# Optimization experiments

Measured on AMD Instinct MI355X. Metric: run time of the kernel, lower is better.

The kernel has to match this reference:

```python
import jax, jax.numpy as jnp
import numpy as np

B, S, D = 2, 2048, 1024
H = 16
HD = D // H  # head_dim = 64


def _xavier(key, shape):
    fan_out, fan_in = shape
    bound = jnp.sqrt(6.0 / (fan_in + fan_out))
    return jax.random.uniform(key, shape, jnp.float32, -bound, bound)


def setup_inputs() -> dict:
    key = jax.random.key(0)
    kx, kqkv, ko = jax.random.split(key, 3)
    x = jax.random.normal(kx, (B, S, D), jnp.float32)
    # torch nn.Linear stores weight as [out, in]; we keep that layout and use x @ W.T
    W_qkv = _xavier(kqkv, (3 * D, D))
    b_qkv = jnp.zeros((3 * D,), jnp.float32)
    W_o = _xavier(ko, (D, D))
    b_o = jnp.zeros((D,), jnp.float32)
    return {"x": x, "W_qkv": W_qkv, "b_qkv": b_qkv, "W_o": W_o, "b_o": b_o}


def reference(x, W_qkv, b_qkv, W_o, b_o):
    b, s, d = x.shape
    h, hd = H, HD
    # qkv projection: [b, s, 3d]
    qkv = jnp.einsum("bsd,ed->bse", x, W_qkv) + b_qkv
    # [b, s, h, 3*hd] -> [b, h, s, 3*hd]
    qkv = qkv.reshape(b, s, h, 3 * hd).transpose(0, 2, 1, 3)
    q, k, v = jnp.split(qkv, 3, axis=-1)
    scale = 1.0 / jnp.sqrt(jnp.asarray(hd, x.dtype))
    logits = jnp.einsum("bhqd,bhkd->bhqk", q, k) * scale
    attn = jax.nn.softmax(logits, axis=-1)
    values = jnp.einsum("bhqk,bhkd->bhqd", attn, v)
    values = values.transpose(0, 2, 1, 3).reshape(b, s, d)
    return jnp.einsum("bsd,ed->bse", values, W_o) + b_o
```

## Files before the change

### kernel.cpp

```cpp
#include <hip/hip_runtime.h>

typedef unsigned short u16;
typedef __attribute__((ext_vector_type(8))) short bf16x8;
typedef __attribute__((ext_vector_type(4))) float f32x4;
typedef __attribute__((ext_vector_type(16))) float f32x16;
typedef __attribute__((ext_vector_type(4))) unsigned short u16x4;

__device__ __forceinline__ u16 f2bf(float f) {
    unsigned u = __float_as_uint(f);
    u = u + 0x7FFFu + ((u >> 16) & 1u);
    return (u16)(u >> 16);
}

__device__ __forceinline__ void gload16(const void* g, void* l) {
    __builtin_amdgcn_global_load_lds(
        (const __attribute__((address_space(1))) unsigned int*)g,
        (__attribute__((address_space(3))) unsigned int*)l,
        16, 0, 0);
}

__device__ __forceinline__ f32x4 mfma16(bf16x8 a, bf16x8 b, f32x4 c) {
    return __builtin_amdgcn_mfma_f32_16x16x32_bf16(a, b, c, 0, 0, 0);
}
__device__ __forceinline__ f32x16 mfma32(bf16x8 a, bf16x8 b, f32x16 c) {
    return __builtin_amdgcn_mfma_f32_32x32x16_bf16(a, b, c, 0, 0, 0);
}

__global__ __launch_bounds__(256) void cvt_all(const float* __restrict__ x,
                                               const float* __restrict__ wqkv,
                                               const float* __restrict__ wo,
                                               u16* __restrict__ dst) {
    int i = blockIdx.x * 256 + threadIdx.x;
    float4 v;
    if (i < 1048576)       v = ((const float4*)x)[i];
    else if (i < 1835008)  v = ((const float4*)wqkv)[i - 1048576];
    else                   v = ((const float4*)wo)[i - 1835008];
    u16x4 o = { f2bf(v.x), f2bf(v.y), f2bf(v.z), f2bf(v.w) };
    ((u16x4*)dst)[i] = o;
}

template <int BM, int BN, bool OUT_BF16>
__global__ __launch_bounds__(256) void gemm_bt(const u16* __restrict__ A,
                                               const u16* __restrict__ Bm,
                                               const float* __restrict__ bias,
                                               void* __restrict__ Cp,
                                               int M, int N, int K) {
    constexpr int FM = BM / 32, FN = BN / 32;
    __shared__ u16 As[BM * 64];
    __shared__ u16 Bs[BN * 64];
    const int tid = threadIdx.x, lane = tid & 63, wave = tid >> 6;
    const int wr = wave >> 1, wc = wave & 1;
    const int l15 = lane & 15, l4 = lane >> 4;

    const int nx = gridDim.x, nwg = nx * gridDim.y;
    const int id = blockIdx.y * nx + blockIdx.x;
    const int wg = (id & 7) * (nwg >> 3) + (id >> 3);
    const int m0 = (wg / nx) * BM, n0 = (wg % nx) * BN;

    f32x4 zero = {0.f, 0.f, 0.f, 0.f};
    f32x4 acc[FM][FN];
#pragma unroll
    for (int m = 0; m < FM; ++m)
#pragma unroll
        for (int n = 0; n < FN; ++n) acc[m][n] = zero;

    const int nt = K >> 6;
    for (int t = 0; t < nt; ++t) {
#pragma unroll
        for (int i = 0; i < BM / 32; ++i) {
            int c = i * 256 + tid;
            int r = c >> 3, kc = (c & 7) ^ (r & 7);
            gload16(A + (size_t)(m0 + r) * K + t * 64 + kc * 8,
                    As + (i * 256 + wave * 64) * 8);
        }
#pragma unroll
        for (int i = 0; i < BN / 32; ++i) {
            int c = i * 256 + tid;
            int r = c >> 3, kc = (c & 7) ^ (r & 7);
            gload16(Bm + (size_t)(n0 + r) * K + t * 64 + kc * 8,
                    Bs + (i * 256 + wave * 64) * 8);
        }
        __syncthreads();
#pragma unroll
        for (int kk = 0; kk < 2; ++kk) {
            bf16x8 af[FM], bfr[FN];
#pragma unroll
            for (int m = 0; m < FM; ++m) {
                int row = wr * (BM / 2) + m * 16 + l15;
                int ch = (kk * 4 + l4) ^ (row & 7);
                af[m] = *(const bf16x8*)((const char*)As + row * 128 + ch * 16);
            }
#pragma unroll
            for (int n = 0; n < FN; ++n) {
                int row = wc * (BN / 2) + n * 16 + l15;
                int ch = (kk * 4 + l4) ^ (row & 7);
                bfr[n] = *(const bf16x8*)((const char*)Bs + row * 128 + ch * 16);
            }
#pragma unroll
            for (int m = 0; m < FM; ++m)
#pragma unroll
                for (int n = 0; n < FN; ++n)
                    acc[m][n] = mfma16(af[m], bfr[n], acc[m][n]);
        }
        __syncthreads();
    }
    float bv[FN];
#pragma unroll
    for (int n = 0; n < FN; ++n) bv[n] = bias[n0 + wc * (BN / 2) + n * 16 + l15];
#pragma unroll
    for (int m = 0; m < FM; ++m) {
#pragma unroll
        for (int j = 0; j < 4; ++j) {
            size_t row = (size_t)(m0 + wr * (BM / 2) + m * 16 + l4 * 4 + j);
#pragma unroll
            for (int n = 0; n < FN; ++n) {
                int col = n0 + wc * (BN / 2) + n * 16 + l15;
                float v = acc[m][n][j] + bv[n];
                if (OUT_BF16)
                    ((u16*)Cp)[row * (size_t)N + col] = f2bf(v);
                else
                    ((float*)Cp)[row * (size_t)N + col] = v;
            }
        }
    }
}

__global__ __launch_bounds__(512) void gemm256(const u16* __restrict__ A,
                                               const u16* __restrict__ Bm,
                                               const float* __restrict__ bias,
                                               u16* __restrict__ Cp,
                                               int M, int N, int K) {
    __shared__ __align__(16) char lds[131072];
    const int tid = threadIdx.x, lane = tid & 63, wave = tid >> 6;
    const int wr = wave >> 2, wc = wave & 3;
    const int l15 = lane & 15, l4 = lane >> 4;

    const int nx = gridDim.x, nwg = nx * gridDim.y;
    const int id = blockIdx.y * nx + blockIdx.x;
    const int wg = (id & 7) * (nwg >> 3) + (id >> 3);
    const int m0 = (wg / nx) * 256, n0 = (wg % nx) * 256;

    const u16* asrc[2][2];
    const u16* bsrc[2][2];
#pragma unroll
    for (int q = 0; q < 2; ++q)
#pragma unroll
        for (int r = 0; r < 2; ++r) {
            int c = r * 512 + tid;
            int lr = c >> 3;
            int kc = (c & 7) ^ (lr & 7);
            asrc[q][r] = A  + (size_t)(m0 + lr + (lr & 64) + q * 64) * K + kc * 8;
            bsrc[q][r] = Bm + (size_t)(n0 + lr + (lr & 96) + q * 32) * K + kc * 8;
        }
    const int sd0 = wave * 1024;
    const int sd1 = 8192 + wave * 1024;

    const int roA = (wr * 64 + l15) * 128;
    const int roB = (wc * 32 + l15) * 128;
    int ch16[2];
#pragma unroll
    for (int kk = 0; kk < 2; ++kk) ch16[kk] = ((kk * 4 + l4) ^ (l15 & 7)) * 16;

    f32x4 zero = {0.f, 0.f, 0.f, 0.f};
    f32x4 acc[2][2][4][2];
#pragma unroll
    for (int a = 0; a < 2; ++a)
#pragma unroll
        for (int b = 0; b < 2; ++b)
#pragma unroll
            for (int c = 0; c < 4; ++c)
#pragma unroll
                for (int d = 0; d < 2; ++d) acc[a][b][c][d] = zero;

#define STG_A(q, tt) { char* rb = lds + (((tt) & 1) * 32768) + (q) * 16384;          \
        gload16(asrc[q][0] + (size_t)(tt) * 64, rb + sd0);                            \
        gload16(asrc[q][1] + (size_t)(tt) * 64, rb + sd1); }
#define STG_B(q, tt) { char* rb = lds + 65536 + (((tt) & 1) * 32768) + (q) * 16384;  \
        gload16(bsrc[q][0] + (size_t)(tt) * 64, rb + sd0);                            \
        gload16(bsrc[q][1] + (size_t)(tt) * 64, rb + sd1); }
#define MFMA_PH(MH, NH) {                                                             \
        __builtin_amdgcn_s_setprio(1);                                                \
        _Pragma("unroll")                                                             \
        for (int fm = 0; fm < 4; ++fm)                                                \
            _Pragma("unroll")                                                         \
            for (int fn = 0; fn < 2; ++fn)                                            \
                _Pragma("unroll")                                                     \
                for (int kk = 0; kk < 2; ++kk)                                        \
                    acc[MH][NH][fm][fn] =                                             \
                        mfma16(af[fm][kk], bfr[NH][fn][kk], acc[MH][NH][fm][fn]);     \
        __builtin_amdgcn_s_setprio(0); }

    STG_A(0, 0); STG_B(0, 0); STG_A(1, 0); STG_B(1, 0);
    asm volatile("s_waitcnt vmcnt(4)" ::: "memory");
    asm volatile("s_barrier" ::: "memory");

    bf16x8 af[4][2], bfr[2][2][2];
    const int nt = K >> 6;
    for (int t = 0; t < nt; ++t) {
        const char* Ab = lds + (t & 1) * 32768;
        const char* Bb = lds + 65536 + (t & 1) * 32768;
#pragma unroll
        for (int fm = 0; fm < 4; ++fm)
#pragma unroll
            for (int kk = 0; kk < 2; ++kk)
                af[fm][kk] = *(const bf16x8*)(Ab + roA + fm * 2048 + ch16[kk]);
#pragma unroll
        for (int fn = 0; fn < 2; ++fn)
#pragma unroll
            for (int kk = 0; kk < 2; ++kk)
                bfr[0][fn][kk] = *(const bf16x8*)(Bb + roB + fn * 2048 + ch16[kk]);
        if (t < nt - 1) STG_A(0, t + 1);
        asm volatile("s_barrier" ::: "memory");
        MFMA_PH(0, 0);
        asm volatile("s_barrier" ::: "memory");
#pragma unroll
        for (int fn = 0; fn < 2; ++fn)
#pragma unroll
            for (int kk = 0; kk < 2; ++kk)
                bfr[1][fn][kk] = *(const bf16x8*)(Bb + 16384 + roB + fn * 2048 + ch16[kk]);
        if (t < nt - 1) STG_B(0, t + 1);
        asm volatile("s_barrier" ::: "memory");
        MFMA_PH(0, 1);
        if (t < nt - 1) asm volatile("s_waitcnt vmcnt(4)" ::: "memory");
        else            asm volatile("s_waitcnt vmcnt(0)" ::: "memory");
        asm volatile("s_barrier" ::: "memory");
#pragma unroll
        for (int fm = 0; fm < 4; ++fm)
#pragma unroll
            for (int kk = 0; kk < 2; ++kk)
                af[fm][kk] = *(const bf16x8*)(Ab + 16384 + roA + fm * 2048 + ch16[kk]);
        if (t < nt - 1) STG_A(1, t + 1);
        asm volatile("s_barrier" ::: "memory");
        MFMA_PH(1, 0);
        asm volatile("s_barrier" ::: "memory");
        if (t < nt - 1) STG_B(1, t + 1);
        asm volatile("s_barrier" ::: "memory");
        MFMA_PH(1, 1);
        if (t < nt - 1) asm volatile("s_waitcnt vmcnt(4)" ::: "memory");
        asm volatile("s_barrier" ::: "memory");
    }
#undef STG_A
#undef STG_B
#undef MFMA_PH

    float bv[2][2];
#pragma unroll
    for (int nh = 0; nh < 2; ++nh)
#pragma unroll
        for (int fn = 0; fn < 2; ++fn)
            bv[nh][fn] = bias[n0 + wc * 64 + nh * 32 + fn * 16 + l15];
#pragma unroll
    for (int mh = 0; mh < 2; ++mh)
#pragma unroll
        for (int fm = 0; fm < 4; ++fm)
#pragma unroll
            for (int j = 0; j < 4; ++j) {
                size_t row = (size_t)(m0 + wr * 128 + mh * 64 + fm * 16 + l4 * 4 + j);
#pragma unroll
                for (int nh = 0; nh < 2; ++nh)
#pragma unroll
                    for (int fn = 0; fn < 2; ++fn) {
                        int col = n0 + wc * 64 + nh * 32 + fn * 16 + l15;
                        Cp[row * (size_t)N + col] =
                            f2bf(acc[mh][nh][fm][fn][j] + bv[nh][fn]);
                    }
            }
}

__global__ __launch_bounds__(256) void transpose_v(const u16* __restrict__ qkv,
                                                   u16* __restrict__ Vt) {
    __shared__ u16 tle[64][65];
    const int s0 = blockIdx.x * 64, h = blockIdx.y, b = blockIdx.z;
    const int tid = threadIdx.x;
#pragma unroll
    for (int i = 0; i < 16; ++i) {
        int idx = i * 256 + tid;
        int sk = idx >> 6, d = idx & 63;
        tle[sk][d] = qkv[(size_t)(b * 2048 + s0 + sk) * 3072 + h * 192 + 128 + d];
    }
    __syncthreads();
#pragma unroll
    for (int i = 0; i < 16; ++i) {
        int idx = i * 256 + tid;
        int d = idx >> 6, sk = idx & 63;
        Vt[((size_t)(b * 16 + h) * 64 + d) * 2048 + s0 + sk] = tle[sk][d];
    }
}

__global__ __launch_bounds__(512, 4) void attn_kernel(const u16* __restrict__ qkv,
                                                      const u16* __restrict__ Vt,
                                                      u16* __restrict__ vals) {
    __shared__ __align__(16) char lds[65536];
    const int qt = blockIdx.x, h = blockIdx.y, b = blockIdx.z;
    const int tid = threadIdx.x, lane = tid & 63, wave = tid >> 6;
    const int gtid = tid & 255, qsub = wave & 3, kvh = wave >> 2;
    const int l31 = lane & 31, hi = lane >> 5;
    const float S2E = 0.18033688f;

    const u16* qbase = qkv + (size_t)(b * 2048 + qt * 128 + qsub * 32 + l31) * 3072 + h * 192;
    bf16x8 Qf[4];
#pragma unroll
    for (int ks = 0; ks < 4; ++ks) {
        bf16x8 q = *(const bf16x8*)(qbase + ks * 16 + hi * 8);
#pragma unroll
        for (int j = 0; j < 8; ++j) {
            float f = __uint_as_float(((unsigned)(u16)q[j]) << 16) * S2E;
            q[j] = (short)f2bf(f);
        }
        Qf[ks] = q;
    }

    bf16x8 ones;
#pragma unroll
    for (int j = 0; j < 8; ++j) ones[j] = (short)0x3F80;

    const u16* kp[2];
    const u16* vp[2];
    int dst[2];
#pragma unroll
    for (int i = 0; i < 2; ++i) {
        int c = i * 256 + gtid;
        int fi = c >> 6, dl = c & 63;
        int mm = fi >> 2, ks = fi & 3;
        int row = mm * 32 + (dl & 31);
        int col = ks * 16 + (dl >> 5) * 8;
        kp[i] = qkv + (size_t)(b * 2048 + kvh * 1024 + row) * 3072 + h * 192 + 64 + col;
        vp[i] = Vt + ((size_t)((b * 16 + h) * 64 + row)) * 2048 + kvh * 1024 + col;
        dst[i] = fi * 512;
    }
    u16* Kst = (u16*)lds + kvh * 8192;
    u16* Vst = (u16*)lds + 16384 + kvh * 8192;

    f32x16 accO[2], accL;
#pragma unroll
    for (int md = 0; md < 2; ++md)
#pragma unroll
        for (int r = 0; r < 16; ++r) accO[md][r] = 0.f;
#pragma unroll
    for (int r = 0; r < 16; ++r) accL[r] = 0.f;

    const char* KsL = (const char*)Kst + lane * 16;
    const char* VsL = (const char*)Vst + lane * 16;

#pragma unroll
    for (int i = 0; i < 2; ++i) gload16(kp[i], Kst + dst[i]);
#pragma unroll
    for (int i = 0; i < 2; ++i) gload16(vp[i], Vst + dst[i]);
#pragma unroll
    for (int i = 0; i < 2; ++i) { kp[i] += 64 * 3072; vp[i] += 64; }

    for (int t = 0; t < 16; ++t) {
        if (t < 15) {
            u16* kd = Kst + ((t + 1) & 1) * 4096;
            u16* vd = Vst + ((t + 1) & 1) * 4096;
#pragma unroll
            for (int i = 0; i < 2; ++i) gload16(kp[i], kd + dst[i]);
#pragma unroll
            for (int i = 0; i < 2; ++i) gload16(vp[i], vd + dst[i]);
#pragma unroll
            for (int i = 0; i < 2; ++i) { kp[i] += 64 * 3072; vp[i] += 64; }
            asm volatile("s_waitcnt vmcnt(4)" ::: "memory");
        } else {
            asm volatile("s_waitcnt vmcnt(0)" ::: "memory");
        }
        asm volatile("s_barrier" ::: "memory");

        const char* Kb = KsL + (t & 1) * 8192;
        const char* Vb = VsL + (t & 1) * 8192;

        f32x16 sc[2];
        __builtin_amdgcn_s_setprio(1);
#pragma unroll
        for (int m = 0; m < 2; ++m) {
            f32x16 c;
#pragma unroll
            for (int r = 0; r < 16; ++r) c[r] = 0.f;
#pragma unroll
            for (int ks = 0; ks < 4; ++ks) {
                bf16x8 kf = *(const bf16x8*)(Kb + (m * 4 + ks) * 1024);
                c = mfma32(kf, Qf[ks], c);
            }
            sc[m] = c;
        }
        __builtin_amdgcn_s_setprio(0);

#pragma unroll
        for (int m = 0; m < 2; ++m)
#pragma unroll
            for (int r = 0; r < 16; ++r)
                sc[m][r] = exp2f(sc[m][r]);

        bf16x8 Pf[4];
#pragma unroll
        for (int m = 0; m < 2; ++m) {
            unsigned W0[4], W1[4];
#pragma unroll
            for (int g = 0; g < 4; ++g) {
                asm("v_cvt_pk_bf16_f32 %0, %1, %2"
                    : "=v"(W0[g]) : "v"(sc[m][4 * g + 0]), "v"(sc[m][4 * g + 1]));
                asm("v_cvt_pk_bf16_f32 %0, %1, %2"
                    : "=v"(W1[g]) : "v"(sc[m][4 * g + 2]), "v"(sc[m][4 * g + 3]));
            }
#pragma unroll
            for (int kpair = 0; kpair < 2; ++kpair) {
                unsigned xa = W0[2 * kpair], ya = W0[2 * kpair + 1];
                unsigned xb = W1[2 * kpair], yb = W1[2 * kpair + 1];
                asm volatile("v_permlane32_swap_b32 %0, %1" : "+v"(xa), "+v"(ya));
                asm volatile("v_permlane32_swap_b32 %0, %1" : "+v"(xb), "+v"(yb));
                union { unsigned w[4]; bf16x8 v; } u;
                u.w[0] = xa; u.w[1] = xb; u.w[2] = ya; u.w[3] = yb;
                Pf[2 * m + kpair] = u.v;
            }
        }

        __builtin_amdgcn_s_setprio(1);
#pragma unroll
        for (int md = 0; md < 2; ++md) {
            f32x16 c = accO[md];
#pragma unroll
            for (int ks = 0; ks < 4; ++ks) {
                bf16x8 vf = *(const bf16x8*)(Vb + (md * 4 + ks) * 1024);
                c = mfma32(vf, Pf[ks], c);
            }
            accO[md] = c;
        }
#pragma unroll
        for (int ks = 0; ks < 4; ++ks)
            accL = mfma32(ones, Pf[ks], accL);
        __builtin_amdgcn_s_setprio(0);

        asm volatile("s_barrier" ::: "memory");
    }

    float lt = accL[0];

    float* MO = (float*)lds;
    float* ML = (float*)(lds + 32768);
    __syncthreads();
    if (kvh == 1) {
#pragma unroll
        for (int md = 0; md < 2; ++md)
#pragma unroll
            for (int g = 0; g < 4; ++g) {
                f32x4 w = { accO[md][4 * g + 0], accO[md][4 * g + 1],
                            accO[md][4 * g + 2], accO[md][4 * g + 3] };
                *(f32x4*)&MO[(qsub * 64 + lane) * 32 + md * 16 + 4 * g] = w;
            }
        ML[qsub * 64 + lane] = lt;
    }
    __syncthreads();
    if (kvh == 0) {
        float inv = 1.f / (lt + ML[qsub * 64 + lane]);
        size_t rowoff = (size_t)(b * 2048 + qt * 128 + qsub * 32 + l31) * 1024 + h * 64;
#pragma unroll
        for (int md = 0; md < 2; ++md)
#pragma unroll
            for (int g = 0; g < 4; ++g) {
                f32x4 w = *(const f32x4*)&MO[(qsub * 64 + lane) * 32 + md * 16 + 4 * g];
                u16x4 o = { f2bf((accO[md][4 * g + 0] + w[0]) * inv),
                            f2bf((accO[md][4 * g + 1] + w[1]) * inv),
                            f2bf((accO[md][4 * g + 2] + w[2]) * inv),
                            f2bf((accO[md][4 * g + 3] + w[3]) * inv) };
                *(u16x4*)(vals + rowoff + md * 32 + 8 * g + 4 * hi) = o;
            }
    }
}

extern "C" void kernel_launch(void* const* d_in, const int* in_sizes, int n_in,
                              void* d_out, int out_size, void* d_ws, size_t ws_size,
                              hipStream_t stream) {
    const float* x    = (const float*)d_in[0];
    const float* Wqkv = (const float*)d_in[1];
    const float* bqkv = (const float*)d_in[2];
    const float* Wo   = (const float*)d_in[3];
    const float* bo   = (const float*)d_in[4];
    float* out = (float*)d_out;

    char* ws = (char*)d_ws;
    u16* x_bf    = (u16*)(ws);
    u16* Wqkv_bf = (u16*)(ws + 8388608);
    u16* Wo_bf   = (u16*)(ws + 14680064);
    u16* qkv_bf  = (u16*)(ws + 16777216);
    u16* Vt      = (u16*)(ws + 41943040);
    u16* vals    = (u16*)(ws + 50331648);

    cvt_all<<<8192, 256, 0, stream>>>(x, Wqkv, Wo, x_bf);

    gemm256<<<dim3(12, 16), 512, 0, stream>>>(x_bf, Wqkv_bf, bqkv, qkv_bf,
                                              4096, 3072, 1024);

    transpose_v<<<dim3(32, 16, 2), 256, 0, stream>>>(qkv_bf, Vt);

    attn_kernel<<<dim3(16, 16, 2), 512, 0, stream>>>(qkv_bf, Vt, vals);

    gemm_bt<128, 64, false><<<dim3(16, 32), 256, 0, stream>>>(vals, Wo_bf, bo,
                                                              (void*)out, 4096, 1024, 1024);
}
```

Baseline: 128.2 us.

## Software-pipeline attention loop: defer PV matmul one tile, triple-buffer V

Restructures the attention main loop so each iteration computes QK^T and exp for the current KV tile, then runs the PV and row-sum MFMAs for the previous tile's probabilities. V staging moves to a three-slot ring, and the wait and barrier move to the end of the iteration. The aim is to overlap exp, conversion and permute work with matrix-core work and to hide load latency better. It raises LDS use from 64KB to 80KB per block, which may limit blocks per CU, and keeps an extra set of P fragments live in registers.

```diff
diff --git a/kernel.cpp b/kernel.cpp
--- a/kernel.cpp
+++ b/kernel.cpp
@@ -290,7 +290,7 @@
 __global__ __launch_bounds__(512, 4) void attn_kernel(const u16* __restrict__ qkv,
                                                       const u16* __restrict__ Vt,
                                                       u16* __restrict__ vals) {
-    __shared__ __align__(16) char lds[65536];
+    __shared__ __align__(16) char lds[81920];
     const int qt = blockIdx.x, h = blockIdx.y, b = blockIdx.z;
     const int tid = threadIdx.x, lane = tid & 63, wave = tid >> 6;
     const int gtid = tid & 255, qsub = wave & 3, kvh = wave >> 2;
@@ -329,7 +329,7 @@
         dst[i] = fi * 512;
     }
     u16* Kst = (u16*)lds + kvh * 8192;
-    u16* Vst = (u16*)lds + 16384 + kvh * 8192;
+    u16* Vst = (u16*)lds + 16384 + kvh * 12288;
 
     f32x16 accO[2], accL;
 #pragma unroll
@@ -348,25 +348,25 @@
     for (int i = 0; i < 2; ++i) gload16(vp[i], Vst + dst[i]);
 #pragma unroll
     for (int i = 0; i < 2; ++i) { kp[i] += 64 * 3072; vp[i] += 64; }
-
+    asm volatile("s_waitcnt vmcnt(2)" ::: "memory");
+    asm volatile("s_barrier" ::: "memory");
+
+    bf16x8 PfP[4];
+    int vstg = 1, vrd = 0;
     for (int t = 0; t < 16; ++t) {
         if (t < 15) {
             u16* kd = Kst + ((t + 1) & 1) * 4096;
-            u16* vd = Vst + ((t + 1) & 1) * 4096;
+            u16* vd = Vst + vstg * 4096;
 #pragma unroll
             for (int i = 0; i < 2; ++i) gload16(kp[i], kd + dst[i]);
 #pragma unroll
             for (int i = 0; i < 2; ++i) gload16(vp[i], vd + dst[i]);
 #pragma unroll
             for (int i = 0; i < 2; ++i) { kp[i] += 64 * 3072; vp[i] += 64; }
-            asm volatile("s_waitcnt vmcnt(4)" ::: "memory");
-        } else {
-            asm volatile("s_waitcnt vmcnt(0)" ::: "memory");
-        }
-        asm volatile("s_barrier" ::: "memory");
+            vstg = (vstg == 2) ? 0 : vstg + 1;
+        }
 
         const char* Kb = KsL + (t & 1) * 8192;
-        const char* Vb = VsL + (t & 1) * 8192;
 
         f32x16 sc[2];
         __builtin_amdgcn_s_setprio(1);
@@ -390,7 +390,7 @@
             for (int r = 0; r < 16; ++r)
                 sc[m][r] = exp2f(sc[m][r]);
 
-        bf16x8 Pf[4];
+        bf16x8 PfN[4];
 #pragma unroll
         for (int m = 0; m < 2; ++m) {
             unsigned W0[4], W1[4];
@@ -409,10 +409,40 @@
                 asm volatile("v_permlane32_swap_b32 %0, %1" : "+v"(xb), "+v"(yb));
                 union { unsigned w[4]; bf16x8 v; } u;
                 u.w[0] = xa; u.w[1] = xb; u.w[2] = ya; u.w[3] = yb;
-                Pf[2 * m + kpair] = u.v;
-            }
-        }
-
+                PfN[2 * m + kpair] = u.v;
+            }
+        }
+
+        if (t > 0) {
+            const char* Vb = VsL + vrd * 8192;
+            __builtin_amdgcn_s_setprio(1);
+#pragma unroll
+            for (int md = 0; md < 2; ++md) {
+                f32x16 c = accO[md];
+#pragma unroll
+                for (int ks = 0; ks < 4; ++ks) {
+                    bf16x8 vf = *(const bf16x8*)(Vb + (md * 4 + ks) * 1024);
+                    c = mfma32(vf, PfP[ks], c);
+                }
+                accO[md] = c;
+            }
+#pragma unroll
+            for (int ks = 0; ks < 4; ++ks)
+                accL = mfma32(ones, PfP[ks], accL);
+            __builtin_amdgcn_s_setprio(0);
+            vrd = (vrd == 2) ? 0 : vrd + 1;
+        }
+
+#pragma unroll
+        for (int ks = 0; ks < 4; ++ks) PfP[ks] = PfN[ks];
+
+        if (t < 15) asm volatile("s_waitcnt vmcnt(2)" ::: "memory");
+        else        asm volatile("s_waitcnt vmcnt(0)" ::: "memory");
+        asm volatile("s_barrier" ::: "memory");
+    }
+
+    {
+        const char* Vb = VsL + vrd * 8192;
         __builtin_amdgcn_s_setprio(1);
 #pragma unroll
         for (int md = 0; md < 2; ++md) {
@@ -420,16 +450,14 @@
 #pragma unroll
             for (int ks = 0; ks < 4; ++ks) {
                 bf16x8 vf = *(const bf16x8*)(Vb + (md * 4 + ks) * 1024);
-                c = mfma32(vf, Pf[ks], c);
+                c = mfma32(vf, PfP[ks], c);
             }
             accO[md] = c;
         }
 #pragma unroll
         for (int ks = 0; ks < 4; ++ks)
-            accL = mfma32(ones, Pf[ks], accL);
+            accL = mfma32(ones, PfP[ks], accL);
         __builtin_amdgcn_s_setprio(0);
-
-        asm volatile("s_barrier" ::: "memory");
     }
 
     float lt = accL[0];
```

Measured after the change: 151.5 us. 1.18x slower.
